# Kernel optimization log

Measured on AMD Instinct MI355X. Metric: run time of the kernel, lower is better.

The kernel has to match this reference:

```python
import jax, jax.numpy as jnp
import numpy as np

EPS = 1e-6
DN = ('NCHW', 'OIHW', 'NCHW')


def _dw_conv(s, w, dilation, k):
    pad = dilation * (k - 1) // 2
    return jax.lax.conv_general_dilated(
        s, w, window_strides=(1, 1), padding=[(pad, pad), (pad, pad)],
        rhs_dilation=(dilation, dilation), dimension_numbers=DN,
        feature_group_count=4)


def _branch(s, dw_w, pw_w, pw_b, dilation, k):
    h = _dw_conv(s, dw_w, dilation, k)           # [B,4,H,W]
    # pointwise 1x1 conv 4 -> 1
    return jnp.einsum('bchw,oc->bohw', h, pw_w) + pw_b[None, :, None, None]


def setup_inputs() -> dict:
    key = jax.random.key(0)
    ks = jax.random.split(key, 12)
    B, C, H, W = 32, 64, 128, 128
    nb, rh = 3, 8
    d = {}
    d['x'] = jax.random.normal(ks[0], (B, C, H, W), dtype=jnp.float32)
    # branch 0: k=3 d=1; branch 1: k=7 d=1; branch 2: k=7 d=2
    d['dw0'] = jax.random.normal(ks[1], (4, 1, 3, 3), dtype=jnp.float32) * 0.2
    d['dw1'] = jax.random.normal(ks[2], (4, 1, 7, 7), dtype=jnp.float32) * 0.1
    d['dw2'] = jax.random.normal(ks[3], (4, 1, 7, 7), dtype=jnp.float32) * 0.1
    d['pw0_w'] = jax.random.normal(ks[4], (1, 4), dtype=jnp.float32) * 0.5
    d['pw0_b'] = jnp.zeros((1,), dtype=jnp.float32)
    d['pw1_w'] = jax.random.normal(ks[5], (1, 4), dtype=jnp.float32) * 0.5
    d['pw1_b'] = jnp.zeros((1,), dtype=jnp.float32)
    d['pw2_w'] = jax.random.normal(ks[6], (1, 4), dtype=jnp.float32) * 0.5
    d['pw2_b'] = jnp.zeros((1,), dtype=jnp.float32)
    # router: 1x1 convs on pooled [B,4,1,1] == dense layers
    d['rw1'] = jax.random.normal(ks[7], (rh, 4), dtype=jnp.float32) * 0.5
    d['rb1'] = jnp.zeros((rh,), dtype=jnp.float32)
    d['rw2'] = jax.random.normal(ks[8], (nb, rh), dtype=jnp.float32) * 0.3
    d['rb2'] = jnp.zeros((nb,), dtype=jnp.float32)
    # t_raw = softplus_inverse(1.0)
    d['t_raw'] = jnp.asarray(np.log(np.expm1(1.0)), dtype=jnp.float32)
    return d


def reference(x, dw0, dw1, dw2, pw0_w, pw0_b, pw1_w, pw1_b, pw2_w, pw2_b,
              rw1, rb1, rw2, rb2, t_raw):
    B, C, H, W = x.shape
    avg_map = jnp.mean(x, axis=1, keepdims=True)        # [B,1,H,W]
    max_map = jnp.max(x, axis=1, keepdims=True)         # [B,1,H,W]
    xs = jnp.linspace(-1.0, 1.0, W, dtype=x.dtype)
    ys = jnp.linspace(-1.0, 1.0, H, dtype=x.dtype)
    yy, xx = jnp.meshgrid(ys, xs, indexing='ij')
    xg = jnp.broadcast_to(xx[None, None], (B, 1, H, W))
    yg = jnp.broadcast_to(yy[None, None], (B, 1, H, W))
    s = jnp.concatenate([avg_map, max_map, xg, yg], axis=1)  # [B,4,H,W]

    # router: global avg pool -> 1x1 conv -> relu -> 1x1 conv -> softmax
    pooled = jnp.mean(s, axis=(2, 3))                    # [B,4]
    hid = jax.nn.relu(pooled @ rw1.T + rb1)              # [B,rh]
    logits = hid @ rw2.T + rb2                           # [B,nb]
    rw = jax.nn.softmax(logits, axis=1)                  # [B,nb]

    z = jnp.stack([
        _branch(s, dw0, pw0_w, pw0_b, 1, 3),
        _branch(s, dw1, pw1_w, pw1_b, 1, 7),
        _branch(s, dw2, pw2_w, pw2_b, 2, 7),
    ], axis=1)                                           # [B,nb,1,H,W]

    wlogits = jnp.sum(rw[:, :, None, None, None] * z, axis=1)  # [B,1,H,W]
    T = jax.nn.softplus(t_raw) + EPS
    sa = jax.nn.sigmoid(wlogits / T)                     # [B,1,H,W]
    Y = x * sa                                           # [B,C,H,W]
    return (Y, sa)
```

## Files before the change

kernel.cpp:

```cpp
#include <hip/hip_runtime.h>

#define B_ 32
#define C_ 64
#define H_ 128
#define W_ 128
#define HW_ (H_*W_)
#define CHW_ (C_*HW_)

__global__ __launch_bounds__(256) void k0_zpos(
    const float* __restrict__ dw0, const float* __restrict__ dw1,
    const float* __restrict__ dw2,
    const float* __restrict__ pw0w, const float* __restrict__ pw0b,
    const float* __restrict__ pw1w, const float* __restrict__ pw1b,
    const float* __restrict__ pw2w, const float* __restrict__ pw2b,
    float* __restrict__ zpos)
{
    int p = blockIdx.x * 256 + threadIdx.x;
    int gy = p >> 7, gx = p & 127;
    const float sc = 2.0f / 127.0f;
    float z0 = pw0b[0], z1 = pw1b[0], z2 = pw2b[0];
    float px0 = pw0w[2], py0 = pw0w[3];
    float px1 = pw1w[2], py1 = pw1w[3];
    float px2 = pw2w[2], py2 = pw2w[3];

    #pragma unroll
    for (int ky = 0; ky < 3; ++ky)
    #pragma unroll
    for (int kx = 0; kx < 3; ++kx) {
        int iy = gy + ky - 1, ix = gx + kx - 1;
        bool ok = ((unsigned)iy < H_) && ((unsigned)ix < W_);
        float xv = ok ? ix * sc - 1.0f : 0.0f;
        float yv = ok ? iy * sc - 1.0f : 0.0f;
        int t = ky * 3 + kx;
        z0 += px0 * dw0[18 + t] * xv + py0 * dw0[27 + t] * yv;
    }
    #pragma unroll
    for (int ky = 0; ky < 7; ++ky)
    #pragma unroll
    for (int kx = 0; kx < 7; ++kx) {
        int iy = gy + ky - 3, ix = gx + kx - 3;
        bool ok = ((unsigned)iy < H_) && ((unsigned)ix < W_);
        float xv = ok ? ix * sc - 1.0f : 0.0f;
        float yv = ok ? iy * sc - 1.0f : 0.0f;
        int t = ky * 7 + kx;
        z1 += px1 * dw1[98 + t] * xv + py1 * dw1[147 + t] * yv;
    }
    #pragma unroll
    for (int ky = 0; ky < 7; ++ky)
    #pragma unroll
    for (int kx = 0; kx < 7; ++kx) {
        int iy = gy + (ky - 3) * 2, ix = gx + (kx - 3) * 2;
        bool ok = ((unsigned)iy < H_) && ((unsigned)ix < W_);
        float xv = ok ? ix * sc - 1.0f : 0.0f;
        float yv = ok ? iy * sc - 1.0f : 0.0f;
        int t = ky * 7 + kx;
        z2 += px2 * dw2[98 + t] * xv + py2 * dw2[147 + t] * yv;
    }
    zpos[p]           = z0;
    zpos[HW_ + p]     = z1;
    zpos[2 * HW_ + p] = z2;
}

__global__ __launch_bounds__(256) void k1_reduce(
    const float* __restrict__ x, float* __restrict__ avgmap,
    float* __restrict__ maxmap, float* __restrict__ partial)
{
    int t = blockIdx.x * 256 + threadIdx.x;
    int base = t * 4;
    int b = base >> 14;
    int q = base & (HW_ - 1);
    const float4* xp = (const float4*)(x + (size_t)b * CHW_ + q);
    float4 v = xp[0];
    float4 s = v, m = v;
    #pragma unroll 8
    for (int c = 1; c < C_; ++c) {
        float4 u = xp[c * (HW_ / 4)];
        s.x += u.x; s.y += u.y; s.z += u.z; s.w += u.w;
        m.x = fmaxf(m.x, u.x); m.y = fmaxf(m.y, u.y);
        m.z = fmaxf(m.z, u.z); m.w = fmaxf(m.w, u.w);
    }
    const float inv = 1.0f / C_;
    float4 a = make_float4(s.x * inv, s.y * inv, s.z * inv, s.w * inv);
    ((float4*)avgmap)[t] = a;
    ((float4*)maxmap)[t] = m;

    float la = a.x + a.y + a.z + a.w;
    float lm = m.x + m.y + m.z + m.w;
    #pragma unroll
    for (int o = 32; o > 0; o >>= 1) {
        la += __shfl_down(la, o);
        lm += __shfl_down(lm, o);
    }
    __shared__ float wa[4], wm[4];
    int lane = threadIdx.x & 63, wid = threadIdx.x >> 6;
    if (lane == 0) { wa[wid] = la; wm[wid] = lm; }
    __syncthreads();
    if (threadIdx.x == 0) {
        partial[2 * blockIdx.x]     = wa[0] + wa[1] + wa[2] + wa[3];
        partial[2 * blockIdx.x + 1] = wm[0] + wm[1] + wm[2] + wm[3];
    }
}

__global__ void k2_router(const float* __restrict__ partial,
                          const float* __restrict__ rw1, const float* __restrict__ rb1,
                          const float* __restrict__ rw2, const float* __restrict__ rb2,
                          const float* __restrict__ t_raw,
                          float* __restrict__ rwout)
{
    int b = threadIdx.x;
    if (b >= B_) return;
    if (b == 0)
        rwout[96] = 1.0f / (log1pf(expf(t_raw[0])) + 1e-6f);
    float s0 = 0.0f, s1 = 0.0f;
    #pragma unroll
    for (int i = 0; i < 16; ++i) {
        s0 += partial[2 * (b * 16 + i)];
        s1 += partial[2 * (b * 16 + i) + 1];
    }
    float p0 = s0 * (1.0f / HW_);
    float p1 = s1 * (1.0f / HW_);
    float hid[8];
    #pragma unroll
    for (int j = 0; j < 8; ++j)
        hid[j] = fmaxf(0.0f, rb1[j] + rw1[j * 4] * p0 + rw1[j * 4 + 1] * p1);
    float lg[3];
    #pragma unroll
    for (int i = 0; i < 3; ++i) {
        float acc = rb2[i];
        #pragma unroll
        for (int j = 0; j < 8; ++j) acc += hid[j] * rw2[i * 8 + j];
        lg[i] = acc;
    }
    float mx = fmaxf(lg[0], fmaxf(lg[1], lg[2]));
    float e0 = expf(lg[0] - mx), e1 = expf(lg[1] - mx), e2 = expf(lg[2] - mx);
    float inv = 1.0f / (e0 + e1 + e2);
    rwout[b * 3 + 0] = e0 * inv;
    rwout[b * 3 + 1] = e1 * inv;
    rwout[b * 3 + 2] = e2 * inv;
}

__global__ __launch_bounds__(512) void k34_branches_apply(
    const float* __restrict__ x,
    const float* __restrict__ avgmap, const float* __restrict__ maxmap,
    const float* __restrict__ dw0, const float* __restrict__ dw1,
    const float* __restrict__ dw2,
    const float* __restrict__ pw0w, const float* __restrict__ pw1w,
    const float* __restrict__ pw2w,
    const float* __restrict__ zpos, const float* __restrict__ rw,
    float* __restrict__ y, float* __restrict__ sa_out)
{
    __shared__ float sA[16][140];
    __shared__ float sM[16][140];
    __shared__ float wA0[9], wM0[9];
    __shared__ float wA1[49], wM1[49], wA2[49], wM2[49];
    __shared__ __align__(16) float ssa[512];

    int b  = blockIdx.y;
    int y0 = blockIdx.x * 4;
    int tix = threadIdx.x;
    const float* am = avgmap + (size_t)b * HW_;
    const float* mm = maxmap + (size_t)b * HW_;

    {
        int r = tix >> 5, c4 = tix & 31;
        int gy = y0 - 6 + r;
        bool ok = (unsigned)gy < H_;
        float4 av = ok ? ((const float4*)(am + gy * W_))[c4]
                       : make_float4(0.f, 0.f, 0.f, 0.f);
        float4 mv = ok ? ((const float4*)(mm + gy * W_))[c4]
                       : make_float4(0.f, 0.f, 0.f, 0.f);
        float* pa = &sA[r][6 + c4 * 4];
        float* pm = &sM[r][6 + c4 * 4];
        pa[0] = av.x; pa[1] = av.y; pa[2] = av.z; pa[3] = av.w;
        pm[0] = mv.x; pm[1] = mv.y; pm[2] = mv.z; pm[3] = mv.w;
    }
    if (tix < 16 * 12) {
        int r = tix / 12, c = tix % 12;
        int cc = (c < 6) ? c : (134 + c - 6);
        sA[r][cc] = 0.0f;
        sM[r][cc] = 0.0f;
    }
    if (tix < 9)  { wA0[tix] = pw0w[0] * dw0[tix];
                    wM0[tix] = pw0w[1] * dw0[9 + tix]; }
    if (tix < 49) { wA1[tix] = pw1w[0] * dw1[tix];
                    wM1[tix] = pw1w[1] * dw1[49 + tix];
                    wA2[tix] = pw2w[0] * dw2[tix];
                    wM2[tix] = pw2w[1] * dw2[49 + tix]; }
    __syncthreads();

    int ly = tix >> 7;
    int lx = tix & 127;
    int gy = y0 + ly;
    int pidx = gy * W_ + lx;

    float z0 = zpos[pidx];
    float z1 = zpos[HW_ + pidx];
    float z2 = zpos[2 * HW_ + pidx];

    #pragma unroll
    for (int ky = 0; ky < 7; ++ky) {
        const float* ra = &sA[ly + 3 + ky][lx + 3];
        const float* rm = &sM[ly + 3 + ky][lx + 3];
        float av[7], mv[7];
        #pragma unroll
        for (int j = 0; j < 7; ++j) { av[j] = ra[j]; mv[j] = rm[j]; }
        #pragma unroll
        for (int j = 0; j < 7; ++j) {
            int t = ky * 7 + j;
            z1 += wA1[t] * av[j] + wM1[t] * mv[j];
        }
        if (ky >= 2 && ky <= 4) {
            #pragma unroll
            for (int j = 2; j <= 4; ++j) {
                int t = (ky - 2) * 3 + (j - 2);
                z0 += wA0[t] * av[j] + wM0[t] * mv[j];
            }
        }
    }
    #pragma unroll
    for (int ky = 0; ky < 7; ++ky) {
        const float* ra = &sA[ly + 2 * ky][lx];
        const float* rm = &sM[ly + 2 * ky][lx];
        #pragma unroll
        for (int kx = 0; kx < 7; ++kx) {
            int t = ky * 7 + kx;
            z2 += wA2[t] * ra[2 * kx] + wM2[t] * rm[2 * kx];
        }
    }

    float wl = rw[b * 3] * z0 + rw[b * 3 + 1] * z1 + rw[b * 3 + 2] * z2;
    float s = 1.0f / (1.0f + expf(-wl * rw[96]));
    ssa[tix] = s;
    sa_out[(size_t)b * HW_ + pidx] = s;
    __syncthreads();

    int wid  = tix >> 6;
    int lane = tix & 63;
    float4 sv0 = ((const float4*)ssa)[lane];
    float4 sv1 = ((const float4*)ssa)[64 + lane];
    const float* xt = x + (size_t)b * CHW_ + y0 * W_;
    float*       yt = y + (size_t)b * CHW_ + y0 * W_;
    #pragma unroll 4
    for (int k = 0; k < 8; ++k) {
        int c = wid + k * 8;
        const float4* xp = (const float4*)(xt + c * HW_);
        float4*       yp = (float4*)(yt + c * HW_);
        float4 a0 = xp[lane];
        float4 a1 = xp[64 + lane];
        yp[lane]      = make_float4(a0.x * sv0.x, a0.y * sv0.y,
                                    a0.z * sv0.z, a0.w * sv0.w);
        yp[64 + lane] = make_float4(a1.x * sv1.x, a1.y * sv1.y,
                                    a1.z * sv1.z, a1.w * sv1.w);
    }
}

extern "C" void kernel_launch(void* const* d_in, const int* in_sizes, int n_in,
                              void* d_out, int out_size, void* d_ws, size_t ws_size,
                              hipStream_t stream)
{
    const float* x     = (const float*)d_in[0];
    const float* dw0   = (const float*)d_in[1];
    const float* dw1   = (const float*)d_in[2];
    const float* dw2   = (const float*)d_in[3];
    const float* pw0w  = (const float*)d_in[4];
    const float* pw0b  = (const float*)d_in[5];
    const float* pw1w  = (const float*)d_in[6];
    const float* pw1b  = (const float*)d_in[7];
    const float* pw2w  = (const float*)d_in[8];
    const float* pw2b  = (const float*)d_in[9];
    const float* rw1   = (const float*)d_in[10];
    const float* rb1   = (const float*)d_in[11];
    const float* rw2   = (const float*)d_in[12];
    const float* rb2   = (const float*)d_in[13];
    const float* t_raw = (const float*)d_in[14];

    float* ws      = (float*)d_ws;
    float* avgmap  = ws;
    float* maxmap  = ws + 524288;
    float* partial = ws + 1048576;
    float* rw      = ws + 1049600;
    float* zpos    = ws + 1049728;

    float* Y  = (float*)d_out;
    float* sa = Y + (size_t)B_ * CHW_;

    k0_zpos<<<HW_ / 256, 256, 0, stream>>>(
        dw0, dw1, dw2, pw0w, pw0b, pw1w, pw1b, pw2w, pw2b, zpos);
    k1_reduce<<<B_ * HW_ / 4 / 256, 256, 0, stream>>>(x, avgmap, maxmap, partial);
    k2_router<<<1, 64, 0, stream>>>(partial, rw1, rb1, rw2, rb2, t_raw, rw);

    dim3 g34(H_ / 4, B_);
    k34_branches_apply<<<g34, 512, 0, stream>>>(
        x, avgmap, maxmap, dw0, dw1, dw2,
        pw0w, pw1w, pw2w, zpos, rw, Y, sa);
}
```

Measured before the change: 334.4 us.

## Split fused conv+apply kernel into separate conv and streaming apply kernels

The fused branch-conv and x*sa apply kernel becomes two kernels. A conv kernel of 256 threads computes two rows per block and writes sa. A separate streaming kernel reads sa and scales x over 16 channels per block, using nontemporal stores. This is meant to give the memory-bound apply phase its own grid, free of the conv's shared-memory and sync overhead. The cost is an extra launch and a round trip of sa through global memory.

New measurement: 320.1 us. 4.3% less time.

```diff
diff --git a/kernel.cpp b/kernel.cpp
--- a/kernel.cpp
+++ b/kernel.cpp
@@ -6,6 +6,8 @@
 #define W_ 128
 #define HW_ (H_*W_)
 #define CHW_ (C_*HW_)
+
+typedef float f4 __attribute__((ext_vector_type(4)));
 
 __global__ __launch_bounds__(256) void k0_zpos(
     const float* __restrict__ dw0, const float* __restrict__ dw1,
@@ -139,30 +141,28 @@
     rwout[b * 3 + 2] = e2 * inv;
 }
 
-__global__ __launch_bounds__(512) void k34_branches_apply(
-    const float* __restrict__ x,
+__global__ __launch_bounds__(256) void k3_conv(
     const float* __restrict__ avgmap, const float* __restrict__ maxmap,
     const float* __restrict__ dw0, const float* __restrict__ dw1,
     const float* __restrict__ dw2,
     const float* __restrict__ pw0w, const float* __restrict__ pw1w,
     const float* __restrict__ pw2w,
     const float* __restrict__ zpos, const float* __restrict__ rw,
-    float* __restrict__ y, float* __restrict__ sa_out)
-{
-    __shared__ float sA[16][140];
-    __shared__ float sM[16][140];
+    float* __restrict__ sa_out)
+{
+    __shared__ float sA[14][140];
+    __shared__ float sM[14][140];
     __shared__ float wA0[9], wM0[9];
     __shared__ float wA1[49], wM1[49], wA2[49], wM2[49];
-    __shared__ __align__(16) float ssa[512];
 
     int b  = blockIdx.y;
-    int y0 = blockIdx.x * 4;
+    int y0 = blockIdx.x * 2;
     int tix = threadIdx.x;
     const float* am = avgmap + (size_t)b * HW_;
     const float* mm = maxmap + (size_t)b * HW_;
 
-    {
-        int r = tix >> 5, c4 = tix & 31;
+    for (int idx = tix; idx < 14 * 32; idx += 256) {
+        int r = idx >> 5, c4 = idx & 31;
         int gy = y0 - 6 + r;
         bool ok = (unsigned)gy < H_;
         float4 av = ok ? ((const float4*)(am + gy * W_))[c4]
@@ -174,8 +174,8 @@
         pa[0] = av.x; pa[1] = av.y; pa[2] = av.z; pa[3] = av.w;
         pm[0] = mv.x; pm[1] = mv.y; pm[2] = mv.z; pm[3] = mv.w;
     }
-    if (tix < 16 * 12) {
-        int r = tix / 12, c = tix % 12;
+    for (int idx = tix; idx < 14 * 12; idx += 256) {
+        int r = idx / 12, c = idx % 12;
         int cc = (c < 6) ? c : (134 + c - 6);
         sA[r][cc] = 0.0f;
         sM[r][cc] = 0.0f;
@@ -230,27 +230,28 @@
 
     float wl = rw[b * 3] * z0 + rw[b * 3 + 1] * z1 + rw[b * 3 + 2] * z2;
     float s = 1.0f / (1.0f + expf(-wl * rw[96]));
-    ssa[tix] = s;
     sa_out[(size_t)b * HW_ + pidx] = s;
-    __syncthreads();
-
-    int wid  = tix >> 6;
-    int lane = tix & 63;
-    float4 sv0 = ((const float4*)ssa)[lane];
-    float4 sv1 = ((const float4*)ssa)[64 + lane];
-    const float* xt = x + (size_t)b * CHW_ + y0 * W_;
-    float*       yt = y + (size_t)b * CHW_ + y0 * W_;
+}
+
+__global__ __launch_bounds__(256) void k4_apply(
+    const float* __restrict__ x, const float* __restrict__ sa,
+    float* __restrict__ y)
+{
+    int tile = blockIdx.x;
+    int cg   = blockIdx.y;
+    int b  = tile >> 4;
+    int p4 = (tile & 15) * 256 + threadIdx.x;
+
+    f4 sv = ((const f4*)(sa + (size_t)b * HW_))[p4];
+    const f4* xb = (const f4*)(x + (size_t)b * CHW_) + p4;
+    f4*       yb = (f4*)(y + (size_t)b * CHW_) + p4;
+
     #pragma unroll 4
-    for (int k = 0; k < 8; ++k) {
-        int c = wid + k * 8;
-        const float4* xp = (const float4*)(xt + c * HW_);
-        float4*       yp = (float4*)(yt + c * HW_);
-        float4 a0 = xp[lane];
-        float4 a1 = xp[64 + lane];
-        yp[lane]      = make_float4(a0.x * sv0.x, a0.y * sv0.y,
-                                    a0.z * sv0.z, a0.w * sv0.w);
-        yp[64 + lane] = make_float4(a1.x * sv1.x, a1.y * sv1.y,
-                                    a1.z * sv1.z, a1.w * sv1.w);
+    for (int k = 0; k < 16; ++k) {
+        int c = cg * 16 + k;
+        f4 v = xb[c * (HW_ / 4)];
+        f4 r = v * sv;
+        __builtin_nontemporal_store(r, &yb[c * (HW_ / 4)]);
     }
 }
 
@@ -289,8 +290,10 @@
     k1_reduce<<<B_ * HW_ / 4 / 256, 256, 0, stream>>>(x, avgmap, maxmap, partial);
     k2_router<<<1, 64, 0, stream>>>(partial, rw1, rb1, rw2, rb2, t_raw, rw);
 
-    dim3 g34(H_ / 4, B_);
-    k34_branches_apply<<<g34, 512, 0, stream>>>(
-        x, avgmap, maxmap, dw0, dw1, dw2,
-        pw0w, pw1w, pw2w, zpos, rw, Y, sa);
-}
+    dim3 g3(H_ / 2, B_);
+    k3_conv<<<g3, 256, 0, stream>>>(
+        avgmap, maxmap, dw0, dw1, dw2, pw0w, pw1w, pw2w, zpos, rw, sa);
+
+    dim3 g4(B_ * HW_ / 4 / 256, 4);
+    k4_apply<<<g4, 256, 0, stream>>>(x, sa, Y);
+}
```
